# Optimization experiments

Hardware: AMD Instinct MI355X
Metric: run time of the kernel (lower is better)

## Reference

```python
import jax, jax.numpy as jnp
import numpy as np

B, L, H, A = 2, 384, 256, 14  # batch, total residues (binder+target), hidden, atoms/residue


def setup_inputs() -> dict:
    key = jax.random.key(0)
    ks = jax.random.split(key, 8)
    s = 1.0 / np.sqrt(H)
    h = jax.random.normal(ks[0], (B, L, H), jnp.float32)          # encoder output
    X = jax.random.normal(ks[1], (B, L, A, 3), jnp.float32)       # coordinates
    mask = jnp.ones((B, L), jnp.int32)                             # residue validity mask
    Wx_w = jax.random.normal(ks[2], (H, H), jnp.float32) * s
    Wx_b = jnp.zeros((H,), jnp.float32)
    Ux_w = jax.random.normal(ks[3], (H, H), jnp.float32) * s
    Ux_b = jnp.zeros((H,), jnp.float32)
    Tx_w = jax.random.normal(ks[4], (A, H), jnp.float32) * s
    Tx_b = jnp.zeros((A,), jnp.float32)
    return dict(h=h, X=X, mask=mask, Wx_w=Wx_w, Wx_b=Wx_b,
                Ux_w=Ux_w, Ux_b=Ux_b, Tx_w=Tx_w, Tx_b=Tx_b)


def reference(h, X, mask, Wx_w, Wx_b, Ux_w, Ux_b, Tx_w, Tx_b):
    # One recurrent coordinate-update step of FADocker._forward.
    m = mask.astype(h.dtype)                                   # (B, L)
    hw = h @ Wx_w.T + Wx_b                                     # (B, L, H)  = W_x(h)
    hu = h @ Ux_w.T + Ux_b                                     # (B, L, H)  = U_x(h)
    mij = hw[:, :, None, :] + hu[:, None, :, :]                # (B, L, L, H)
    gate = jnp.einsum('bijh,ah->bija', jax.nn.relu(mij), Tx_w) + Tx_b  # (B, L, L, A) = T_x(mij)
    xij = (X[:, :, None] - X[:, None, :]) * gate[..., None]   # (B, L, L, A, 3)
    f = jnp.einsum('bijac,bj->biac', xij, m)                   # masked sum over j
    f = f / (1e-6 + m.sum(axis=1)[:, None, None, None])        # (B, L, A, 3)
    return X + jnp.clip(f, -20.0, 20.0)
```

## Files before the change

### kernel.cpp

```cpp
#include <hip/hip_runtime.h>
#include <hip/hip_bf16.h>

#define HDIM 256
#define LDIM 384
#define BDIM 2
#define ADIM 14

typedef __attribute__((ext_vector_type(8))) short bf16x8;
typedef __attribute__((ext_vector_type(4))) float f32x4;

static __device__ __forceinline__ unsigned pack_bf16(float x, float y) {
    __hip_bfloat162 t = __float22bfloat162_rn(make_float2(x, y));
    return *reinterpret_cast<unsigned*>(&t);
}

__global__ __launch_bounds__(256) void k_gemm(
    const float* __restrict__ h,
    const float* __restrict__ Wx_w, const float* __restrict__ Wx_b,
    const float* __restrict__ Ux_w, const float* __restrict__ Ux_b,
    float* __restrict__ hw, unsigned* __restrict__ huP)
{
    __shared__ float hsT[32][34];
    __shared__ float wsT[32][34];
    const int t  = threadIdx.x;
    const int tx = t & 15, ty = t >> 4;
    const int row0 = blockIdx.y * 32;
    const int col0 = blockIdx.x * 32;

    const int lr = t & 31;
    const int lk = (t >> 5) * 4;
    const float* __restrict__ hrow = &h[(row0 + lr) * HDIM];
    const int c_l = col0 + lr;
    const float* __restrict__ wrow = (c_l < HDIM) ? &Wx_w[c_l * HDIM]
                                                  : &Ux_w[(c_l - HDIM) * HDIM];

    float a00 = 0.f, a01 = 0.f, a10 = 0.f, a11 = 0.f;

    for (int k0 = 0; k0 < HDIM; k0 += 32) {
        const float4 hv = *(const float4*)&hrow[k0 + lk];
        const float4 wv = *(const float4*)&wrow[k0 + lk];
        hsT[lk + 0][lr] = hv.x; hsT[lk + 1][lr] = hv.y;
        hsT[lk + 2][lr] = hv.z; hsT[lk + 3][lr] = hv.w;
        wsT[lk + 0][lr] = wv.x; wsT[lk + 1][lr] = wv.y;
        wsT[lk + 2][lr] = wv.z; wsT[lk + 3][lr] = wv.w;
        __syncthreads();
        #pragma unroll
        for (int kk = 0; kk < 32; ++kk) {
            const float2 av = *(const float2*)&hsT[kk][ty * 2];
            const float2 bv = *(const float2*)&wsT[kk][tx * 2];
            a00 = fmaf(av.x, bv.x, a00); a01 = fmaf(av.x, bv.y, a01);
            a10 = fmaf(av.y, bv.x, a10); a11 = fmaf(av.y, bv.y, a11);
        }
        __syncthreads();
    }

    const int row = row0 + ty * 2;
    const int b = row / LDIM, i0 = row % LDIM;
    const int c0 = col0 + tx * 2;
    if (c0 < HDIM) {
        const float b0 = Wx_b[c0], b1 = Wx_b[c0 + 1];
        *(float2*)&hw[row * HDIM + c0]       = make_float2(a00 + b0, a01 + b1);
        *(float2*)&hw[(row + 1) * HDIM + c0] = make_float2(a10 + b0, a11 + b1);
    } else {
        const int ch = c0 - HDIM;
        const float b0 = Ux_b[ch], b1 = Ux_b[ch + 1];
        uint2 pv;
        pv.x = pack_bf16(a00 + b0, a01 + b1);
        pv.y = pack_bf16(a10 + b0, a11 + b1);
        *(uint2*)&huP[(b * (HDIM / 2) + (ch >> 1)) * LDIM + i0] = pv;
    }
}

__global__ __launch_bounds__(384) void k_main(
    const float* __restrict__ hw, const unsigned* __restrict__ huP,
    const float* __restrict__ X, const int* __restrict__ mask,
    const float* __restrict__ Tx_w, const float* __restrict__ Tx_b,
    float* __restrict__ out)
{
    __shared__ unsigned TxP[16 * 130];
    __shared__ float m_lds[LDIM];
    __shared__ float part2[24 * 16 * 4];
    __shared__ float part_m[24];

    const int i = blockIdx.x, b = blockIdx.y;
    const int tid = threadIdx.x;
    const int w = tid >> 6;
    const int lane = tid & 63;
    const int n = lane & 15;
    const int quad = lane >> 4;

    for (int idx = tid; idx < 16 * 128; idx += 384) {
        const int nn = idx >> 7, k2 = idx & 127;
        unsigned v = 0;
        if (nn < ADIM) {
            const float2 tw = *(const float2*)&Tx_w[nn * HDIM + 2 * k2];
            v = pack_bf16(tw.x, tw.y);
        }
        TxP[nn * 130 + k2] = v;
    }
    m_lds[tid] = (float)mask[b * LDIM + tid];
    __syncthreads();

    const float* __restrict__ hwrow = &hw[(b * LDIM + i) * HDIM];
    const unsigned* __restrict__ hub = &huP[b * (HDIM / 2) * LDIM];

    f32x4 acc[4];
    #pragma unroll
    for (int t = 0; t < 4; ++t) acc[t] = (f32x4){0.f, 0.f, 0.f, 0.f};

    const int jbase = w * 64 + n;

    #pragma unroll 2
    for (int kc = 0; kc < 8; ++kc) {
        union { unsigned u[4]; bf16x8 v; } bu;
        const int bofs = n * 130 + kc * 16 + quad * 4;
        *(uint2*)&bu.u[0] = *(const uint2*)&TxP[bofs];
        *(uint2*)&bu.u[2] = *(const uint2*)&TxP[bofs + 2];
        const float4 hwa = *(const float4*)(hwrow + kc * 32 + quad * 8);
        const float4 hwb = *(const float4*)(hwrow + kc * 32 + quad * 8 + 4);
        const float hv[8] = {hwa.x, hwa.y, hwa.z, hwa.w, hwb.x, hwb.y, hwb.z, hwb.w};
        const int h2base = kc * 16 + quad * 4;
        #pragma unroll
        for (int t = 0; t < 4; ++t) {
            const unsigned* __restrict__ hp = &hub[h2base * LDIM + jbase + t * 16];
            union { unsigned u[4]; bf16x8 v; } au;
            #pragma unroll
            for (int d = 0; d < 4; ++d) {
                const unsigned pk = hp[d * LDIM];
                const float lo = __uint_as_float(pk << 16);
                const float hi = __uint_as_float(pk & 0xffff0000u);
                const float t0 = fmaxf(hv[2 * d] + lo, 0.f);
                const float t1 = fmaxf(hv[2 * d + 1] + hi, 0.f);
                au.u[d] = pack_bf16(t0, t1);
            }
            acc[t] = __builtin_amdgcn_mfma_f32_16x16x32_bf16(au.v, bu.v, acc[t], 0, 0, 0);
        }
    }

    float s1 = 0.f, s2x = 0.f, s2y = 0.f, s2z = 0.f, pm = 0.f;
    if (n < ADIM) {
        const float txb = Tx_b[n];
        #pragma unroll
        for (int t = 0; t < 4; ++t) {
            #pragma unroll
            for (int r = 0; r < 4; ++r) {
                const int jd = (w * 4 + t) * 16 + quad * 4 + r;
                const float m = m_lds[jd];
                const float g = acc[t][r] + txb;
                const float mg = m * g;
                const float* __restrict__ Xp = &X[((b * LDIM + jd) * ADIM + n) * 3];
                s1 += mg;
                s2x = fmaf(mg, Xp[0], s2x);
                s2y = fmaf(mg, Xp[1], s2y);
                s2z = fmaf(mg, Xp[2], s2z);
                pm += m;
            }
        }
    }
    {
        f32x4 sv = {s2x, s2y, s2z, s1};
        *(f32x4*)&part2[((w * 4 + quad) * 16 + n) * 4] = sv;
    }
    if (n == 0) part_m[w * 4 + quad] = pm;
    __syncthreads();

    if (tid < 42) {
        const int a = tid / 3, c = tid % 3;
        float S2 = 0.f, S1 = 0.f, msum = 0.f;
        #pragma unroll 4
        for (int g = 0; g < 24; ++g) {
            const float* __restrict__ p = &part2[(g * 16 + a) * 4];
            S2 += p[c]; S1 += p[3]; msum += part_m[g];
        }
        const float denom = 1e-6f + msum;
        const int idx = ((b * LDIM + i) * ADIM + a) * 3 + c;
        const float xi = X[idx];
        float f = (xi * S1 - S2) / denom;
        f = fminf(fmaxf(f, -20.f), 20.f);
        out[idx] = xi + f;
    }
}

extern "C" void kernel_launch(void* const* d_in, const int* in_sizes, int n_in,
                              void* d_out, int out_size, void* d_ws, size_t ws_size,
                              hipStream_t stream) {
    (void)in_sizes; (void)n_in; (void)out_size; (void)ws_size;
    const float* h    = (const float*)d_in[0];
    const float* X    = (const float*)d_in[1];
    const int*   mask = (const int*)  d_in[2];
    const float* Wx_w = (const float*)d_in[3];
    const float* Wx_b = (const float*)d_in[4];
    const float* Ux_w = (const float*)d_in[5];
    const float* Ux_b = (const float*)d_in[6];
    const float* Tx_w = (const float*)d_in[7];
    const float* Tx_b = (const float*)d_in[8];
    float* out = (float*)d_out;

    float*    hw  = (float*)d_ws;
    unsigned* huP = (unsigned*)(hw + BDIM * LDIM * HDIM);

    k_gemm<<<dim3(16, 24), dim3(256), 0, stream>>>(h, Wx_w, Wx_b, Ux_w, Ux_b, hw, huP);
    k_main<<<dim3(LDIM, BDIM), 384, 0, stream>>>(hw, huP, X, mask, Tx_w, Tx_b, out);
}
```

Before: 98.51 us.

## Switch to fp16 packed relu-add, MFMA front GEMM, and precomputed Tx fragments

Replaces the bf16 path with fp16. The hw+hu add and relu now run as packed half2 operations on fp16 values stored row-major, so each lane loads a uint4 directly instead of four strided scalar loads plus per-element float conversion. The front GEMM is rewritten to use 16x16x32 f16 MFMA instead of scalar FMA tiling. Packing of Tx_w is moved into an extra block of the front kernel, so the main kernel no longer rebuilds it in LDS for every block. This is meant to cut the ALU conversion work and strided global loads in the hot loop, at the cost of fp16 range and precision for the intermediate activations.

```diff
diff --git a/kernel.cpp b/kernel.cpp
--- a/kernel.cpp
+++ b/kernel.cpp
@@ -1,139 +1,133 @@
 #include <hip/hip_runtime.h>
-#include <hip/hip_bf16.h>
+#include <hip/hip_fp16.h>
 
 #define HDIM 256
 #define LDIM 384
 #define BDIM 2
 #define ADIM 14
 
-typedef __attribute__((ext_vector_type(8))) short bf16x8;
+typedef __attribute__((ext_vector_type(8))) _Float16 f16x8;
+typedef __attribute__((ext_vector_type(2))) _Float16 f16x2;
 typedef __attribute__((ext_vector_type(4))) float f32x4;
 
-static __device__ __forceinline__ unsigned pack_bf16(float x, float y) {
-    __hip_bfloat162 t = __float22bfloat162_rn(make_float2(x, y));
-    return *reinterpret_cast<unsigned*>(&t);
+static __device__ __forceinline__ unsigned pack_f16(float x, float y) {
+    f16x2 t = {(_Float16)x, (_Float16)y};
+    union { f16x2 v; unsigned u; } c; c.v = t;
+    return c.u;
 }
 
-__global__ __launch_bounds__(256) void k_gemm(
+static __device__ __forceinline__ unsigned relu_add(unsigned a, unsigned b) {
+    union { unsigned u; f16x2 v; } ua, ub, ur;
+    ua.u = a; ub.u = b;
+    const f16x2 z = {(_Float16)0.f, (_Float16)0.f};
+    ur.v = __builtin_elementwise_max(ua.v + ub.v, z);
+    return ur.u;
+}
+
+__global__ __launch_bounds__(256) void k_front(
     const float* __restrict__ h,
     const float* __restrict__ Wx_w, const float* __restrict__ Wx_b,
     const float* __restrict__ Ux_w, const float* __restrict__ Ux_b,
-    float* __restrict__ hw, unsigned* __restrict__ huP)
+    const float* __restrict__ Tx_w,
+    unsigned* __restrict__ hwP, unsigned* __restrict__ huP,
+    unsigned* __restrict__ txP)
 {
-    __shared__ float hsT[32][34];
-    __shared__ float wsT[32][34];
-    const int t  = threadIdx.x;
-    const int tx = t & 15, ty = t >> 4;
-    const int row0 = blockIdx.y * 32;
-    const int col0 = blockIdx.x * 32;
+    const int tid = threadIdx.x;
+    if (blockIdx.x == 384) {
+        for (int idx = tid; idx < 16 * 128; idx += 256) {
+            const int a = idx >> 7, k2 = idx & 127;
+            unsigned v = 0;
+            if (a < ADIM) {
+                const float2 tw = *(const float2*)&Tx_w[a * HDIM + 2 * k2];
+                v = pack_f16(tw.x, tw.y);
+            }
+            txP[idx] = v;
+        }
+        return;
+    }
+    const int w = tid >> 6, lane = tid & 63;
+    const int n = lane & 15, quad = lane >> 4;
+    const int g = blockIdx.x * 4 + w;
+    const int ctile = g & 31;
+    const int rtile = g >> 5;
 
-    const int lr = t & 31;
-    const int lk = (t >> 5) * 4;
-    const float* __restrict__ hrow = &h[(row0 + lr) * HDIM];
-    const int c_l = col0 + lr;
-    const float* __restrict__ wrow = (c_l < HDIM) ? &Wx_w[c_l * HDIM]
-                                                  : &Ux_w[(c_l - HDIM) * HDIM];
+    const int arow = (ctile & 15) * 16 + n;
+    const float* __restrict__ Arow = (ctile < 16) ? &Wx_w[arow * HDIM]
+                                                  : &Ux_w[arow * HDIM];
+    const float* __restrict__ Brow = &h[(rtile * 16 + n) * HDIM];
 
-    float a00 = 0.f, a01 = 0.f, a10 = 0.f, a11 = 0.f;
-
-    for (int k0 = 0; k0 < HDIM; k0 += 32) {
-        const float4 hv = *(const float4*)&hrow[k0 + lk];
-        const float4 wv = *(const float4*)&wrow[k0 + lk];
-        hsT[lk + 0][lr] = hv.x; hsT[lk + 1][lr] = hv.y;
-        hsT[lk + 2][lr] = hv.z; hsT[lk + 3][lr] = hv.w;
-        wsT[lk + 0][lr] = wv.x; wsT[lk + 1][lr] = wv.y;
-        wsT[lk + 2][lr] = wv.z; wsT[lk + 3][lr] = wv.w;
-        __syncthreads();
-        #pragma unroll
-        for (int kk = 0; kk < 32; ++kk) {
-            const float2 av = *(const float2*)&hsT[kk][ty * 2];
-            const float2 bv = *(const float2*)&wsT[kk][tx * 2];
-            a00 = fmaf(av.x, bv.x, a00); a01 = fmaf(av.x, bv.y, a01);
-            a10 = fmaf(av.y, bv.x, a10); a11 = fmaf(av.y, bv.y, a11);
-        }
-        __syncthreads();
+    f32x4 acc = {0.f, 0.f, 0.f, 0.f};
+    #pragma unroll
+    for (int kc = 0; kc < 8; ++kc) {
+        const int ko = kc * 32 + quad * 8;
+        const float4 a0 = *(const float4*)&Arow[ko];
+        const float4 a1 = *(const float4*)&Arow[ko + 4];
+        const float4 b0 = *(const float4*)&Brow[ko];
+        const float4 b1 = *(const float4*)&Brow[ko + 4];
+        union { unsigned u[4]; f16x8 v; } af, bf;
+        af.u[0] = pack_f16(a0.x, a0.y); af.u[1] = pack_f16(a0.z, a0.w);
+        af.u[2] = pack_f16(a1.x, a1.y); af.u[3] = pack_f16(a1.z, a1.w);
+        bf.u[0] = pack_f16(b0.x, b0.y); bf.u[1] = pack_f16(b0.z, b0.w);
+        bf.u[2] = pack_f16(b1.x, b1.y); bf.u[3] = pack_f16(b1.z, b1.w);
+        acc = __builtin_amdgcn_mfma_f32_16x16x32_f16(af.v, bf.v, acc, 0, 0, 0);
     }
 
-    const int row = row0 + ty * 2;
-    const int b = row / LDIM, i0 = row % LDIM;
-    const int c0 = col0 + tx * 2;
-    if (c0 < HDIM) {
-        const float b0 = Wx_b[c0], b1 = Wx_b[c0 + 1];
-        *(float2*)&hw[row * HDIM + c0]       = make_float2(a00 + b0, a01 + b1);
-        *(float2*)&hw[(row + 1) * HDIM + c0] = make_float2(a10 + b0, a11 + b1);
-    } else {
-        const int ch = c0 - HDIM;
-        const float b0 = Ux_b[ch], b1 = Ux_b[ch + 1];
-        uint2 pv;
-        pv.x = pack_bf16(a00 + b0, a01 + b1);
-        pv.y = pack_bf16(a10 + b0, a11 + b1);
-        *(uint2*)&huP[(b * (HDIM / 2) + (ch >> 1)) * LDIM + i0] = pv;
-    }
+    const int row = rtile * 16 + n;
+    const int c0 = (ctile & 15) * 16 + quad * 4;
+    const float4 bias = (ctile < 16) ? *(const float4*)&Wx_b[c0]
+                                     : *(const float4*)&Ux_b[c0];
+    uint2 pv;
+    pv.x = pack_f16(acc[0] + bias.x, acc[1] + bias.y);
+    pv.y = pack_f16(acc[2] + bias.z, acc[3] + bias.w);
+    unsigned* __restrict__ dst = (ctile < 16) ? hwP : huP;
+    *(uint2*)&dst[row * 128 + (ctile & 15) * 8 + quad * 2] = pv;
 }
 
 __global__ __launch_bounds__(384) void k_main(
-    const float* __restrict__ hw, const unsigned* __restrict__ huP,
+    const unsigned* __restrict__ hwP, const unsigned* __restrict__ huP,
+    const unsigned* __restrict__ txP,
     const float* __restrict__ X, const int* __restrict__ mask,
-    const float* __restrict__ Tx_w, const float* __restrict__ Tx_b,
+    const float* __restrict__ Tx_b,
     float* __restrict__ out)
 {
-    __shared__ unsigned TxP[16 * 130];
     __shared__ float m_lds[LDIM];
     __shared__ float part2[24 * 16 * 4];
     __shared__ float part_m[24];
 
     const int i = blockIdx.x, b = blockIdx.y;
     const int tid = threadIdx.x;
-    const int w = tid >> 6;
-    const int lane = tid & 63;
-    const int n = lane & 15;
-    const int quad = lane >> 4;
+    const int w = tid >> 6, lane = tid & 63;
+    const int n = lane & 15, quad = lane >> 4;
 
-    for (int idx = tid; idx < 16 * 128; idx += 384) {
-        const int nn = idx >> 7, k2 = idx & 127;
-        unsigned v = 0;
-        if (nn < ADIM) {
-            const float2 tw = *(const float2*)&Tx_w[nn * HDIM + 2 * k2];
-            v = pack_bf16(tw.x, tw.y);
-        }
-        TxP[nn * 130 + k2] = v;
-    }
     m_lds[tid] = (float)mask[b * LDIM + tid];
     __syncthreads();
 
-    const float* __restrict__ hwrow = &hw[(b * LDIM + i) * HDIM];
-    const unsigned* __restrict__ hub = &huP[b * (HDIM / 2) * LDIM];
+    const unsigned* __restrict__ hwr = &hwP[(b * LDIM + i) * 128];
+    const unsigned* __restrict__ hub = &huP[b * LDIM * 128];
+    const unsigned* __restrict__ txr = &txP[n * 128];
 
     f32x4 acc[4];
     #pragma unroll
     for (int t = 0; t < 4; ++t) acc[t] = (f32x4){0.f, 0.f, 0.f, 0.f};
 
-    const int jbase = w * 64 + n;
-
-    #pragma unroll 2
+    #pragma unroll 4
     for (int kc = 0; kc < 8; ++kc) {
-        union { unsigned u[4]; bf16x8 v; } bu;
-        const int bofs = n * 130 + kc * 16 + quad * 4;
-        *(uint2*)&bu.u[0] = *(const uint2*)&TxP[bofs];
-        *(uint2*)&bu.u[2] = *(const uint2*)&TxP[bofs + 2];
-        const float4 hwa = *(const float4*)(hwrow + kc * 32 + quad * 8);
-        const float4 hwb = *(const float4*)(hwrow + kc * 32 + quad * 8 + 4);
-        const float hv[8] = {hwa.x, hwa.y, hwa.z, hwa.w, hwb.x, hwb.y, hwb.z, hwb.w};
-        const int h2base = kc * 16 + quad * 4;
+        const int ko = kc * 16 + quad * 4;
+        const uint4 hw4 = *(const uint4*)&hwr[ko];
+        const uint4 tx4 = *(const uint4*)&txr[ko];
+        union { unsigned u[4]; f16x8 v; } bfrag;
+        bfrag.u[0] = tx4.x; bfrag.u[1] = tx4.y;
+        bfrag.u[2] = tx4.z; bfrag.u[3] = tx4.w;
         #pragma unroll
         for (int t = 0; t < 4; ++t) {
-            const unsigned* __restrict__ hp = &hub[h2base * LDIM + jbase + t * 16];
-            union { unsigned u[4]; bf16x8 v; } au;
-            #pragma unroll
-            for (int d = 0; d < 4; ++d) {
-                const unsigned pk = hp[d * LDIM];
-                const float lo = __uint_as_float(pk << 16);
-                const float hi = __uint_as_float(pk & 0xffff0000u);
-                const float t0 = fmaxf(hv[2 * d] + lo, 0.f);
-                const float t1 = fmaxf(hv[2 * d + 1] + hi, 0.f);
-                au.u[d] = pack_bf16(t0, t1);
-            }
-            acc[t] = __builtin_amdgcn_mfma_f32_16x16x32_bf16(au.v, bu.v, acc[t], 0, 0, 0);
+            const int j = (w * 4 + t) * 16 + n;
+            const uint4 hu4 = *(const uint4*)&hub[j * 128 + ko];
+            union { unsigned u[4]; f16x8 v; } af;
+            af.u[0] = relu_add(hw4.x, hu4.x);
+            af.u[1] = relu_add(hw4.y, hu4.y);
+            af.u[2] = relu_add(hw4.z, hu4.z);
+            af.u[3] = relu_add(hw4.w, hu4.w);
+            acc[t] = __builtin_amdgcn_mfma_f32_16x16x32_f16(af.v, bfrag.v, acc[t], 0, 0, 0);
         }
     }
 
@@ -196,9 +190,10 @@
     const float* Tx_b = (const float*)d_in[8];
     float* out = (float*)d_out;
 
-    float*    hw  = (float*)d_ws;
-    unsigned* huP = (unsigned*)(hw + BDIM * LDIM * HDIM);
+    unsigned* hwP = (unsigned*)d_ws;
+    unsigned* huP = hwP + BDIM * LDIM * (HDIM / 2);
+    unsigned* txP = huP + BDIM * LDIM * (HDIM / 2);
 
-    k_gemm<<<dim3(16, 24), dim3(256), 0, stream>>>(h, Wx_w, Wx_b, Ux_w, Ux_b, hw, huP);
-    k_main<<<dim3(LDIM, BDIM), 384, 0, stream>>>(hw, huP, X, mask, Tx_w, Tx_b, out);
+    k_front<<<385, 256, 0, stream>>>(h, Wx_w, Wx_b, Ux_w, Ux_b, Tx_w, hwP, huP, txP);
+    k_main<<<dim3(LDIM, BDIM), 384, 0, stream>>>(hwP, huP, txP, X, mask, Tx_b, out);
 }
```

New measurement: 102.0 us. 3.5% more time.
